# Performance work log

Hardware: AMD Instinct MI355X
Metric: run time of the kernel (lower is better)

## Reference

```python
import jax, jax.numpy as jnp
import numpy as np

N_NODES = 100000
N_GRAPHS = 64
IN_CH, HID, OUT = 128, 64, 2
N_EDGES = 1600000


def gcn_conv(x, row, col, W, b):
    # PyG GCNConv: h = x @ W; add self-loops; symmetric normalization
    # deg[i] = 1 (self-loop) + in-degree at target nodes (col)
    N = x.shape[0]
    h = x @ W                                            # [N, F_out]
    deg = jnp.ones((N,), h.dtype).at[col].add(1.0)       # [N]
    dinv = jax.lax.rsqrt(deg)                            # deg^{-1/2}
    coef = dinv[row] * dinv[col]                         # [E] edge norm
    msg = h[row] * coef[:, None]                         # gather + scale
    agg = jnp.zeros_like(h).at[col].add(msg)             # scatter-add at targets
    agg = agg + h * (dinv * dinv)[:, None]               # self-loop term
    return agg + b


def setup_inputs() -> dict:
    key = jax.random.key(0)
    k1, k2, k3, k4, k5, k6, k7 = jax.random.split(key, 7)
    x = jax.random.normal(k1, (N_NODES, IN_CH), jnp.float32)
    edge_index = jax.random.randint(k2, (2, N_EDGES), 0, N_NODES, jnp.int64)
    batch = jnp.sort(jax.random.randint(k3, (N_NODES,), 0, N_GRAPHS, jnp.int64))
    s = 1.0 / np.sqrt(IN_CH)
    W1 = jax.random.uniform(k4, (IN_CH, HID), jnp.float32, -s, s)
    b1 = jnp.zeros((HID,), jnp.float32)
    sh = 1.0 / np.sqrt(HID)
    W2 = jax.random.uniform(k5, (HID, HID), jnp.float32, -sh, sh)
    b2 = jnp.zeros((HID,), jnp.float32)
    W3 = jax.random.uniform(k6, (HID, HID), jnp.float32, -sh, sh)
    b3 = jnp.zeros((HID,), jnp.float32)
    Wlin = jax.random.uniform(k7, (HID, OUT), jnp.float32, -sh, sh)
    blin = jnp.zeros((OUT,), jnp.float32)
    return {"x": x, "edge_index": edge_index, "batch": batch,
            "W1": W1, "b1": b1, "W2": W2, "b2": b2, "W3": W3, "b3": b3,
            "Wlin": Wlin, "blin": blin}


def reference(x, edge_index, batch, W1, b1, W2, b2, W3, b3, Wlin, blin):
    row, col = edge_index[0], edge_index[1]
    h = gcn_conv(x, row, col, W1, b1)
    h = jax.nn.relu(h)
    h = gcn_conv(h, row, col, W2, b2)
    h = jax.nn.relu(h)
    h = gcn_conv(h, row, col, W3, b3)    # no relu after last conv
    # global_mean_pool over batch ids
    pooled = jax.ops.segment_sum(h, batch, num_segments=N_GRAPHS)
    counts = jax.ops.segment_sum(jnp.ones((h.shape[0],), h.dtype), batch,
                                 num_segments=N_GRAPHS)
    pooled = pooled / jnp.maximum(counts, 1.0)[:, None]
    # dropout p=0.5 is identity in eval mode
    return pooled @ Wlin + blin          # [N_GRAPHS, OUT]
```

## Files before the change

kernel.cpp:

```cpp
#include <hip/hip_runtime.h>
#include <hip/hip_fp16.h>

#define IN_CH 128
#define HIDDEN 64


__global__ __launch_bounds__(512)
void bucket_hist_kernel(const int* __restrict__ col, int* __restrict__ bhist, int E) {
    __shared__ int h[512];
    h[threadIdx.x] = 0;
    __syncthreads();
    const int start = blockIdx.x * 8192;
    const int end = min(start + 8192, E);
    for (int e = start + threadIdx.x; e < end; e += 512)
        atomicAdd(&h[col[e] >> 8], 1);
    __syncthreads();
    if (h[threadIdx.x]) atomicAdd(&bhist[threadIdx.x], h[threadIdx.x]);
}

__global__ __launch_bounds__(512)
void bucket_scan_kernel(const int* __restrict__ bhist, int* __restrict__ bbase,
                        int* __restrict__ bpos, int* __restrict__ off,
                        int nb, int N, int E) {
    __shared__ int s[512];
    const int t = threadIdx.x;
    const int v = (t < nb) ? bhist[t] : 0;
    s[t] = v;
    __syncthreads();
    for (int d = 1; d < 512; d <<= 1) {
        int u = (t >= d) ? s[t - d] : 0;
        __syncthreads();
        s[t] += u;
        __syncthreads();
    }
    const int b = s[t] - v;
    if (t < nb) { bbase[t] = b; bpos[t] = b; }
    if (t == 0) { bbase[nb] = E; off[N] = E; }
}

__global__ __launch_bounds__(512)
void bucket_scatter_kernel(const int* __restrict__ row, const int* __restrict__ col,
                           int* __restrict__ bpos, unsigned* __restrict__ tmp, int E) {
    __shared__ int h[512];
    __shared__ int base[512];
    h[threadIdx.x] = 0;
    __syncthreads();
    const int start = blockIdx.x * 8192;
    const int end = min(start + 8192, E);
    for (int e = start + threadIdx.x; e < end; e += 512)
        atomicAdd(&h[col[e] >> 8], 1);
    __syncthreads();
    const int i = threadIdx.x;
    base[i] = h[i] ? atomicAdd(&bpos[i], h[i]) : 0;
    h[i] = 0;
    __syncthreads();
    for (int e = start + threadIdx.x; e < end; e += 512) {
        const int c = col[e];
        const int bk = c >> 8;
        const int p = base[bk] + atomicAdd(&h[bk], 1);
        tmp[p] = ((unsigned)row[e] << 8) | (unsigned)(c & 255);
    }
}

__global__ __launch_bounds__(256)
void bucket_sort_kernel(const unsigned* __restrict__ tmp, const int* __restrict__ bbase,
                        int* __restrict__ off, float* __restrict__ dinv,
                        int* __restrict__ srcrow, int N) {
    __shared__ int cnt[256];
    __shared__ int sc[256];
    const int b = blockIdx.x;
    const int node0 = b << 8;
    const int t = threadIdx.x;
    const int lo = bbase[b], hi = bbase[b + 1];
    cnt[t] = 0;
    __syncthreads();
    for (int j = lo + t; j < hi; j += 256)
        atomicAdd(&cnt[tmp[j] & 255u], 1);
    __syncthreads();
    const int v = cnt[t];
    sc[t] = v;
    __syncthreads();
    for (int d = 1; d < 256; d <<= 1) {
        int u = (t >= d) ? sc[t - d] : 0;
        __syncthreads();
        sc[t] += u;
        __syncthreads();
    }
    const int excl = sc[t] - v;
    const int node = node0 + t;
    if (node < N) {
        off[node] = lo + excl;
        dinv[node] = rsqrtf((float)v + 1.0f);
    }
    cnt[t] = lo + excl;
    __syncthreads();
    for (int j = lo + t; j < hi; j += 256) {
        const unsigned pk = tmp[j];
        const int p = atomicAdd(&cnt[pk & 255u], 1);
        srcrow[p] = (int)(pk >> 8);
    }
}


template <int K>
__global__ __launch_bounds__(256)
void gemm_kernel(const float* __restrict__ X, const float* __restrict__ W,
                 const float* __restrict__ dinv, __half* __restrict__ Hs, int N) {
    constexpr int BK = 16;
    __shared__ float xs[BK][64];
    __shared__ float ws[BK][64];
    const int tid  = threadIdx.x;
    const int row0 = blockIdx.x * 64;
    const int tx4  = (tid & 15) << 2;
    const int ty4  = (tid >> 4) << 2;
    const int lrow = tid >> 2;
    const int kq   = (tid & 3) << 2;
    const int wk   = tid >> 4;
    const int wc   = (tid & 15) << 2;
    int grow = row0 + lrow;
    if (grow >= N) grow = N - 1;

    float acc[4][4] = {};
    for (int k0 = 0; k0 < K; k0 += BK) {
        const float4 xv = *reinterpret_cast<const float4*>(&X[(size_t)grow * K + k0 + kq]);
        const float4 wv = *reinterpret_cast<const float4*>(&W[(size_t)(k0 + wk) * 64 + wc]);
        __syncthreads();
        xs[kq + 0][lrow] = xv.x;
        xs[kq + 1][lrow] = xv.y;
        xs[kq + 2][lrow] = xv.z;
        xs[kq + 3][lrow] = xv.w;
        *reinterpret_cast<float4*>(&ws[wk][wc]) = wv;
        __syncthreads();
#pragma unroll
        for (int k = 0; k < BK; ++k) {
            const float4 a = *reinterpret_cast<const float4*>(&xs[k][ty4]);
            const float4 b = *reinterpret_cast<const float4*>(&ws[k][tx4]);
            const float av[4] = {a.x, a.y, a.z, a.w};
            const float bv[4] = {b.x, b.y, b.z, b.w};
#pragma unroll
            for (int r = 0; r < 4; ++r)
#pragma unroll
                for (int c = 0; c < 4; ++c)
                    acc[r][c] = fmaf(av[r], bv[c], acc[r][c]);
        }
    }
#pragma unroll
    for (int r = 0; r < 4; ++r) {
        int n = row0 + ty4 + r;
        if (n < N) {
            const float dn = dinv[n];
            union { uint2 u; __half2 h2[2]; } pk;
            pk.h2[0] = __floats2half2_rn(acc[r][0] * dn, acc[r][1] * dn);
            pk.h2[1] = __floats2half2_rn(acc[r][2] * dn, acc[r][3] * dn);
            *reinterpret_cast<uint2*>(&Hs[(size_t)n * 64 + tx4]) = pk.u;
        }
    }
}


template <bool RELU>
__global__ __launch_bounds__(256)
void gather_kernel(const __half* __restrict__ Hs, const float* __restrict__ dinv,
                   const int* __restrict__ off, const int* __restrict__ srcrow,
                   const float* __restrict__ bias, float* __restrict__ A, int N) {
    const int tid  = threadIdx.x;
    const int lane = tid & 63;
    const int q    = lane >> 4;
    const int fl   = (lane & 15) << 2;
    const int wid  = tid >> 6;
    const int c    = blockIdx.x * 16 + wid * 4 + q;
    const int cc   = (c < N) ? c : N - 1;
    const int lo = off[cc], hi = off[cc + 1];

    float4 acc = make_float4(0.f, 0.f, 0.f, 0.f);
    int j = lo;
    while (__any(j < hi)) {
        int idx[8];
#pragma unroll
        for (int u = 0; u < 8; ++u) {
            const int jj = j + u;
            idx[u] = srcrow[jj < hi ? jj : (hi > lo ? hi - 1 : 0)];
        }
        uint2 hv[8];
#pragma unroll
        for (int u = 0; u < 8; ++u)
            hv[u] = *reinterpret_cast<const uint2*>(&Hs[(size_t)idx[u] * 64 + fl]);
#pragma unroll
        for (int u = 0; u < 8; ++u) {
            if (j + u < hi) {
                union { uint2 uu; __half2 h2[2]; } v; v.uu = hv[u];
                const float2 a = __half22float2(v.h2[0]);
                const float2 b = __half22float2(v.h2[1]);
                acc.x += a.x; acc.y += a.y; acc.z += b.x; acc.w += b.y;
            }
        }
        j += 8;
    }

    if (c < N) {
        const float dc = dinv[c];
        union { uint2 uu; __half2 h2[2]; } sv;
        sv.uu = *reinterpret_cast<const uint2*>(&Hs[(size_t)c * 64 + fl]);
        const float2 s0 = __half22float2(sv.h2[0]);
        const float2 s1 = __half22float2(sv.h2[1]);
        const float4 bl = *reinterpret_cast<const float4*>(&bias[fl]);
        float4 o;
        o.x = dc * (acc.x + s0.x) + bl.x;
        o.y = dc * (acc.y + s0.y) + bl.y;
        o.z = dc * (acc.z + s1.x) + bl.z;
        o.w = dc * (acc.w + s1.y) + bl.w;
        if (RELU) {
            o.x = fmaxf(o.x, 0.f); o.y = fmaxf(o.y, 0.f);
            o.z = fmaxf(o.z, 0.f); o.w = fmaxf(o.w, 0.f);
        }
        *reinterpret_cast<float4*>(&A[(size_t)c * 64 + fl]) = o;
    }
}


__global__ __launch_bounds__(256)
void pool_kernel(const float* __restrict__ A, const int* __restrict__ batch,
                 float* __restrict__ pooled, int* __restrict__ gcnt, int N) {
    const int g = blockIdx.x >> 3;
    const int stripe = blockIdx.x & 7;
    int lo = 0, hi = N;
    while (lo < hi) { int m = (lo + hi) >> 1; if (batch[m] < g) lo = m + 1; else hi = m; }
    const int beg = lo;
    lo = beg; hi = N;
    while (lo < hi) { int m = (lo + hi) >> 1; if (batch[m] < g + 1) lo = m + 1; else hi = m; }
    const int end = lo;

    const int lane = threadIdx.x & 63;
    const int wsid = stripe * 4 + (threadIdx.x >> 6);
    float acc = 0.f;
    for (int i = beg + wsid; i < end; i += 32)
        acc += A[(size_t)i * 64 + lane];
    atomicAdd(&pooled[g * 64 + lane], acc);
    if (stripe == 0 && threadIdx.x == 0) gcnt[g] = end - beg;
}

__global__ void final_kernel(const float* __restrict__ pooled, const int* __restrict__ gcnt,
                             const float* __restrict__ Wlin, const float* __restrict__ blin,
                             float* __restrict__ out) {
    const int t = threadIdx.x;
    const int g = t >> 1, o = t & 1;
    const float c = (float)max(gcnt[g], 1);
    float acc = 0.f;
    for (int k = 0; k < 64; ++k)
        acc = fmaf(pooled[g * 64 + k], Wlin[k * 2 + o], acc);
    out[g * 2 + o] = acc / c + blin[o];
}


extern "C" void kernel_launch(void* const* d_in, const int* in_sizes, int n_in,
                              void* d_out, int out_size, void* d_ws, size_t ws_size,
                              hipStream_t stream) {
    const float* x     = (const float*)d_in[0];
    const int*   ei    = (const int*)d_in[1];
    const int*   batch = (const int*)d_in[2];
    const float* W1    = (const float*)d_in[3];
    const float* b1    = (const float*)d_in[4];
    const float* W2    = (const float*)d_in[5];
    const float* b2    = (const float*)d_in[6];
    const float* W3    = (const float*)d_in[7];
    const float* b3    = (const float*)d_in[8];
    const float* Wlin  = (const float*)d_in[9];
    const float* blin  = (const float*)d_in[10];

    const int N = in_sizes[0] / IN_CH;
    const int E = in_sizes[1] / 2;
    const int* row = ei;
    const int* col = ei + E;
    const int nb = (N + 255) >> 8;

    char* p = (char*)d_ws;
    auto alloc = [&](size_t bytes) {
        char* q = p;
        p += (bytes + 511) & ~(size_t)511;
        return q;
    };
    int*      off    = (int*)alloc((size_t)(N + 1) * 4);
    float*    dinv   = (float*)alloc((size_t)N * 4);
    int*      srcrow = (int*)alloc((size_t)E * 4);
    unsigned* tmp    = (unsigned*)alloc((size_t)E * 4);
    __half*   Hbuf   = (__half*)alloc((size_t)N * HIDDEN * 2);
    float*    Abuf   = (float*)alloc((size_t)N * HIDDEN * 4);
    int*      bhist  = (int*)alloc(512 * 4);
    int*      bbase  = (int*)alloc(513 * 4);
    int*      bpos   = (int*)alloc(512 * 4);
    float*    pooled = (float*)alloc(64 * 64 * 4);
    int*      gcnt   = (int*)alloc(64 * 4);
    (void)ws_size; (void)n_in; (void)out_size;

    hipMemsetAsync(bhist, 0, 512 * 4, stream);
    const int eb = (E + 8191) / 8192;
    bucket_hist_kernel<<<eb, 512, 0, stream>>>(col, bhist, E);
    bucket_scan_kernel<<<1, 512, 0, stream>>>(bhist, bbase, bpos, off, nb, N, E);
    bucket_scatter_kernel<<<eb, 512, 0, stream>>>(row, col, bpos, tmp, E);
    bucket_sort_kernel<<<nb, 256, 0, stream>>>(tmp, bbase, off, dinv, srcrow, N);

    const int gemm_grid   = (N + 63) / 64;
    const int gather_grid = (N + 15) / 16;
    gemm_kernel<IN_CH><<<gemm_grid, 256, 0, stream>>>(x, W1, dinv, Hbuf, N);
    gather_kernel<true><<<gather_grid, 256, 0, stream>>>(Hbuf, dinv, off, srcrow, b1, Abuf, N);
    gemm_kernel<HIDDEN><<<gemm_grid, 256, 0, stream>>>(Abuf, W2, dinv, Hbuf, N);
    gather_kernel<true><<<gather_grid, 256, 0, stream>>>(Hbuf, dinv, off, srcrow, b2, Abuf, N);
    gemm_kernel<HIDDEN><<<gemm_grid, 256, 0, stream>>>(Abuf, W3, dinv, Hbuf, N);
    gather_kernel<false><<<gather_grid, 256, 0, stream>>>(Hbuf, dinv, off, srcrow, b3, Abuf, N);

    hipMemsetAsync(pooled, 0, 64 * 64 * 4, stream);
    pool_kernel<<<512, 256, 0, stream>>>(Abuf, batch, pooled, gcnt, N);
    final_kernel<<<1, 128, 0, stream>>>(pooled, gcnt, Wlin, blin, (float*)d_out);
}
```

Before: 335.0 us.

## Use fp16 MFMA for node GEMMs and store intermediate activations in fp16

Replaces the shared-memory fp32 FMA GEMM with a wave-level MFMA 16x16x32 f16 kernel that reads pre-packed fp16 weights and loads A rows directly without LDS staging. The gather kernel now writes layer outputs as fp16, which halves activation traffic for the following GEMM and pool reads. Three small pack kernels are added to convert weights into MFMA operand layout. The risk is lower precision in intermediate activations, extra launches, and scattered 2-byte stores in the GEMM epilogue.

```diff
diff --git a/kernel.cpp b/kernel.cpp
--- a/kernel.cpp
+++ b/kernel.cpp
@@ -3,6 +3,9 @@
 
 #define IN_CH 128
 #define HIDDEN 64
+
+typedef _Float16 half8 __attribute__((ext_vector_type(8)));
+typedef float f32x4 __attribute__((ext_vector_type(4)));
 
 
 __global__ __launch_bounds__(512)
@@ -102,57 +105,72 @@
 }
 
 
-template <int K>
+__global__ void pack_kernel(const float* __restrict__ W, _Float16* __restrict__ Wp, int K) {
+    const int tid = threadIdx.x;
+    const int l = tid & 63;
+    const int g = tid >> 6;
+    const int kb = (l >> 4) * 8;
+    const int c = 16 * g + (l & 15);
+    for (int s = 0; s < K / 32; ++s) {
+        half8 v;
+#pragma unroll
+        for (int j = 0; j < 8; ++j)
+            v[j] = (_Float16)W[(size_t)(32 * s + kb + j) * 64 + c];
+        *reinterpret_cast<half8*>(&Wp[((size_t)(s * 4 + g) * 64 + l) * 8]) = v;
+    }
+}
+
+
+template <int K, bool AF32>
 __global__ __launch_bounds__(256)
-void gemm_kernel(const float* __restrict__ X, const float* __restrict__ W,
-                 const float* __restrict__ dinv, __half* __restrict__ Hs, int N) {
-    constexpr int BK = 16;
-    __shared__ float xs[BK][64];
-    __shared__ float ws[BK][64];
-    const int tid  = threadIdx.x;
-    const int row0 = blockIdx.x * 64;
-    const int tx4  = (tid & 15) << 2;
-    const int ty4  = (tid >> 4) << 2;
-    const int lrow = tid >> 2;
-    const int kq   = (tid & 3) << 2;
-    const int wk   = tid >> 4;
-    const int wc   = (tid & 15) << 2;
-    int grow = row0 + lrow;
-    if (grow >= N) grow = N - 1;
-
-    float acc[4][4] = {};
-    for (int k0 = 0; k0 < K; k0 += BK) {
-        const float4 xv = *reinterpret_cast<const float4*>(&X[(size_t)grow * K + k0 + kq]);
-        const float4 wv = *reinterpret_cast<const float4*>(&W[(size_t)(k0 + wk) * 64 + wc]);
-        __syncthreads();
-        xs[kq + 0][lrow] = xv.x;
-        xs[kq + 1][lrow] = xv.y;
-        xs[kq + 2][lrow] = xv.z;
-        xs[kq + 3][lrow] = xv.w;
-        *reinterpret_cast<float4*>(&ws[wk][wc]) = wv;
-        __syncthreads();
-#pragma unroll
-        for (int k = 0; k < BK; ++k) {
-            const float4 a = *reinterpret_cast<const float4*>(&xs[k][ty4]);
-            const float4 b = *reinterpret_cast<const float4*>(&ws[k][tx4]);
-            const float av[4] = {a.x, a.y, a.z, a.w};
-            const float bv[4] = {b.x, b.y, b.z, b.w};
-#pragma unroll
-            for (int r = 0; r < 4; ++r)
-#pragma unroll
-                for (int c = 0; c < 4; ++c)
-                    acc[r][c] = fmaf(av[r], bv[c], acc[r][c]);
-        }
-    }
-#pragma unroll
-    for (int r = 0; r < 4; ++r) {
-        int n = row0 + ty4 + r;
-        if (n < N) {
-            const float dn = dinv[n];
-            union { uint2 u; __half2 h2[2]; } pk;
-            pk.h2[0] = __floats2half2_rn(acc[r][0] * dn, acc[r][1] * dn);
-            pk.h2[1] = __floats2half2_rn(acc[r][2] * dn, acc[r][3] * dn);
-            *reinterpret_cast<uint2*>(&Hs[(size_t)n * 64 + tx4]) = pk.u;
+void gemm_mfma_kernel(const void* __restrict__ Aptr, const _Float16* __restrict__ Wp,
+                      const float* __restrict__ dinv, _Float16* __restrict__ Hs, int N) {
+    const int tid = threadIdx.x;
+    const int l = tid & 63;
+    const int w = tid >> 6;
+    const int r0 = blockIdx.x * 64 + w * 16;
+    const int arow_ = r0 + (l & 15);
+    const int arow = arow_ < N ? arow_ : N - 1;
+    const int kb = (l >> 4) * 8;
+
+    f32x4 acc[4] = {};
+#pragma unroll
+    for (int s = 0; s < K / 32; ++s) {
+        half8 a;
+        if constexpr (AF32) {
+            const float* A = (const float*)Aptr;
+            const float4 f0 = *reinterpret_cast<const float4*>(&A[(size_t)arow * K + 32 * s + kb]);
+            const float4 f1 = *reinterpret_cast<const float4*>(&A[(size_t)arow * K + 32 * s + kb + 4]);
+            a[0] = (_Float16)f0.x; a[1] = (_Float16)f0.y;
+            a[2] = (_Float16)f0.z; a[3] = (_Float16)f0.w;
+            a[4] = (_Float16)f1.x; a[5] = (_Float16)f1.y;
+            a[6] = (_Float16)f1.z; a[7] = (_Float16)f1.w;
+        } else {
+            const _Float16* A = (const _Float16*)Aptr;
+            a = *reinterpret_cast<const half8*>(&A[(size_t)arow * K + 32 * s + kb]);
+        }
+        const half8* Wb = reinterpret_cast<const half8*>(&Wp[(size_t)(s * 4) * 64 * 8]);
+#pragma unroll
+        for (int g = 0; g < 4; ++g) {
+            const half8 b = Wb[g * 64 + l];
+            acc[g] = __builtin_amdgcn_mfma_f32_16x16x32_f16(a, b, acc[g], 0, 0, 0);
+        }
+    }
+
+    const int rb = r0 + (l >> 4) * 4;
+    float dv[4];
+#pragma unroll
+    for (int j = 0; j < 4; ++j) {
+        const int r = rb + j;
+        dv[j] = dinv[r < N ? r : N - 1];
+    }
+#pragma unroll
+    for (int g = 0; g < 4; ++g) {
+#pragma unroll
+        for (int j = 0; j < 4; ++j) {
+            const int r = rb + j;
+            if (r < N)
+                Hs[(size_t)r * 64 + g * 16 + (l & 15)] = (_Float16)(acc[g][j] * dv[j]);
         }
     }
 }
@@ -162,7 +180,7 @@
 __global__ __launch_bounds__(256)
 void gather_kernel(const __half* __restrict__ Hs, const float* __restrict__ dinv,
                    const int* __restrict__ off, const int* __restrict__ srcrow,
-                   const float* __restrict__ bias, float* __restrict__ A, int N) {
+                   const float* __restrict__ bias, __half* __restrict__ A, int N) {
     const int tid  = threadIdx.x;
     const int lane = tid & 63;
     const int q    = lane >> 4;
@@ -213,13 +231,16 @@
             o.x = fmaxf(o.x, 0.f); o.y = fmaxf(o.y, 0.f);
             o.z = fmaxf(o.z, 0.f); o.w = fmaxf(o.w, 0.f);
         }
-        *reinterpret_cast<float4*>(&A[(size_t)c * 64 + fl]) = o;
+        union { uint2 uu; __half2 h2[2]; } ov;
+        ov.h2[0] = __floats2half2_rn(o.x, o.y);
+        ov.h2[1] = __floats2half2_rn(o.z, o.w);
+        *reinterpret_cast<uint2*>(&A[(size_t)c * 64 + fl]) = ov.uu;
     }
 }
 
 
 __global__ __launch_bounds__(256)
-void pool_kernel(const float* __restrict__ A, const int* __restrict__ batch,
+void pool_kernel(const __half* __restrict__ A, const int* __restrict__ batch,
                  float* __restrict__ pooled, int* __restrict__ gcnt, int N) {
     const int g = blockIdx.x >> 3;
     const int stripe = blockIdx.x & 7;
@@ -234,7 +255,7 @@
     const int wsid = stripe * 4 + (threadIdx.x >> 6);
     float acc = 0.f;
     for (int i = beg + wsid; i < end; i += 32)
-        acc += A[(size_t)i * 64 + lane];
+        acc += __half2float(A[(size_t)i * 64 + lane]);
     atomicAdd(&pooled[g * 64 + lane], acc);
     if (stripe == 0 && threadIdx.x == 0) gcnt[g] = end - beg;
 }
@@ -283,8 +304,11 @@
     float*    dinv   = (float*)alloc((size_t)N * 4);
     int*      srcrow = (int*)alloc((size_t)E * 4);
     unsigned* tmp    = (unsigned*)alloc((size_t)E * 4);
-    __half*   Hbuf   = (__half*)alloc((size_t)N * HIDDEN * 2);
-    float*    Abuf   = (float*)alloc((size_t)N * HIDDEN * 4);
+    _Float16* Hbuf   = (_Float16*)alloc((size_t)N * HIDDEN * 2);
+    _Float16* Abuf   = (_Float16*)alloc((size_t)N * HIDDEN * 2);
+    _Float16* Wp1    = (_Float16*)alloc((size_t)IN_CH * 64 * 2);
+    _Float16* Wp2    = (_Float16*)alloc((size_t)HIDDEN * 64 * 2);
+    _Float16* Wp3    = (_Float16*)alloc((size_t)HIDDEN * 64 * 2);
     int*      bhist  = (int*)alloc(512 * 4);
     int*      bbase  = (int*)alloc(513 * 4);
     int*      bpos   = (int*)alloc(512 * 4);
@@ -299,16 +323,20 @@
     bucket_scatter_kernel<<<eb, 512, 0, stream>>>(row, col, bpos, tmp, E);
     bucket_sort_kernel<<<nb, 256, 0, stream>>>(tmp, bbase, off, dinv, srcrow, N);
 
+    pack_kernel<<<1, 256, 0, stream>>>(W1, Wp1, IN_CH);
+    pack_kernel<<<1, 256, 0, stream>>>(W2, Wp2, HIDDEN);
+    pack_kernel<<<1, 256, 0, stream>>>(W3, Wp3, HIDDEN);
+
     const int gemm_grid   = (N + 63) / 64;
     const int gather_grid = (N + 15) / 16;
-    gemm_kernel<IN_CH><<<gemm_grid, 256, 0, stream>>>(x, W1, dinv, Hbuf, N);
-    gather_kernel<true><<<gather_grid, 256, 0, stream>>>(Hbuf, dinv, off, srcrow, b1, Abuf, N);
-    gemm_kernel<HIDDEN><<<gemm_grid, 256, 0, stream>>>(Abuf, W2, dinv, Hbuf, N);
-    gather_kernel<true><<<gather_grid, 256, 0, stream>>>(Hbuf, dinv, off, srcrow, b2, Abuf, N);
-    gemm_kernel<HIDDEN><<<gemm_grid, 256, 0, stream>>>(Abuf, W3, dinv, Hbuf, N);
-    gather_kernel<false><<<gather_grid, 256, 0, stream>>>(Hbuf, dinv, off, srcrow, b3, Abuf, N);
+    gemm_mfma_kernel<IN_CH, true><<<gemm_grid, 256, 0, stream>>>(x, Wp1, dinv, Hbuf, N);
+    gather_kernel<true><<<gather_grid, 256, 0, stream>>>((const __half*)Hbuf, dinv, off, srcrow, b1, (__half*)Abuf, N);
+    gemm_mfma_kernel<HIDDEN, false><<<gemm_grid, 256, 0, stream>>>(Abuf, Wp2, dinv, Hbuf, N);
+    gather_kernel<true><<<gather_grid, 256, 0, stream>>>((const __half*)Hbuf, dinv, off, srcrow, b2, (__half*)Abuf, N);
+    gemm_mfma_kernel<HIDDEN, false><<<gemm_grid, 256, 0, stream>>>(Abuf, Wp3, dinv, Hbuf, N);
+    gather_kernel<false><<<gather_grid, 256, 0, stream>>>((const __half*)Hbuf, dinv, off, srcrow, b3, (__half*)Abuf, N);
 
     hipMemsetAsync(pooled, 0, 64 * 64 * 4, stream);
-    pool_kernel<<<512, 256, 0, stream>>>(Abuf, batch, pooled, gcnt, N);
+    pool_kernel<<<512, 256, 0, stream>>>((const __half*)Abuf, batch, pooled, gcnt, N);
     final_kernel<<<1, 128, 0, stream>>>(pooled, gcnt, Wlin, blin, (float*)d_out);
 }
```

New measurement: 314.0 us. -6.3%, faster.
